# Kernel optimization log

Hardware: AMD Instinct MI355X
Metric: run time of the kernel (lower is better)

The kernel has to match this reference:

```python
import jax, jax.numpy as jnp
import numpy as np

N_NODES = 50000
IN_CH = 128
OUT_CH = 64
N_EDGES = 800000


def setup_inputs() -> dict:
    key = jax.random.key(0)
    k1, k2, k3, k4 = jax.random.split(key, 4)
    z = jax.random.normal(k1, (N_NODES, IN_CH), dtype=jnp.float32)
    edge_index = jax.random.randint(k2, (2, N_EDGES), 0, N_NODES, dtype=jnp.int64)
    # GCNConv params: weight [in, out] (glorot-ish), bias [out]
    W = jax.random.normal(k3, (IN_CH, OUT_CH), dtype=jnp.float32) / np.sqrt(IN_CH)
    b = jnp.zeros((OUT_CH,), dtype=jnp.float32)
    return {"z": z, "edge_index": edge_index, "W": W, "b": b}


def reference(z, edge_index, W, b):
    N = z.shape[0]
    # linear transform first (out_channels < in_channels reduces message traffic)
    x = z @ W  # [N, out]
    # add self-loops
    loop = jnp.arange(N, dtype=edge_index.dtype)
    src = jnp.concatenate([edge_index[0], loop])
    dst = jnp.concatenate([edge_index[1], loop])
    # symmetric normalization deg^-1/2 (degree counted on dst, incl. self-loops)
    deg = jnp.zeros((N,), dtype=x.dtype).at[dst].add(1.0)
    dinv = jnp.where(deg > 0, jax.lax.rsqrt(deg), 0.0)
    norm = dinv[src] * dinv[dst]  # [E+N]
    msg = x[src] * norm[:, None]  # gather + scale
    out = jax.ops.segment_sum(msg, dst, num_segments=N)  # scatter-add
    return jax.nn.relu(out + b)
```

## Files before the change

### kernel.cpp

```cpp
#include <hip/hip_runtime.h>
#include <hip/hip_bf16.h>

#define IN_CH 128
#define OUT_CH 64

#define CSHIFT 6
#define BNODES 64
#define NCMAX 1024
#define CAP 1536
#define BIN_EPT 8

typedef __attribute__((ext_vector_type(8))) short bf16x8;
typedef __attribute__((ext_vector_type(4))) float f32x4;

__device__ inline short f2bfs(float x) {
    __hip_bfloat16 h = __float2bfloat16(x);
    return __builtin_bit_cast(short, h);
}
__device__ inline float bf2f(unsigned short h) {
    unsigned int u = ((unsigned int)h) << 16;
    return __builtin_bit_cast(float, u);
}

__global__ void bin_edges(const int* __restrict__ ei, int* __restrict__ gctr,
                          unsigned int* __restrict__ ebuf, int E, int NC) {
    __shared__ int cnt[NCMAX];
    __shared__ int gbase[NCMAX];
    for (int i = threadIdx.x; i < NC; i += blockDim.x) cnt[i] = 0;
    __syncthreads();

    unsigned int pk[BIN_EPT];
    int bk[BIN_EPT];
    const int g0 = (blockIdx.x * blockDim.x + threadIdx.x) * BIN_EPT;

    if (g0 + BIN_EPT <= E) {
        int4 s0 = *(const int4*)(ei + g0);
        int4 s1 = *(const int4*)(ei + g0 + 4);
        int4 d0 = *(const int4*)(ei + E + g0);
        int4 d1 = *(const int4*)(ei + E + g0 + 4);
        int ss[BIN_EPT] = {s0.x, s0.y, s0.z, s0.w, s1.x, s1.y, s1.z, s1.w};
        int dd[BIN_EPT] = {d0.x, d0.y, d0.z, d0.w, d1.x, d1.y, d1.z, d1.w};
#pragma unroll
        for (int k = 0; k < BIN_EPT; ++k) {
            pk[k] = ((unsigned int)dd[k] << 16) | (unsigned int)ss[k];
            bk[k] = dd[k] >> CSHIFT;
            atomicAdd(&cnt[bk[k]], 1);
        }
    } else {
#pragma unroll
        for (int k = 0; k < BIN_EPT; ++k) {
            int e = g0 + k;
            if (e < E) {
                int s = ei[e];
                int d = ei[E + e];
                pk[k] = ((unsigned int)d << 16) | (unsigned int)s;
                bk[k] = d >> CSHIFT;
                atomicAdd(&cnt[bk[k]], 1);
            } else bk[k] = -1;
        }
    }
    __syncthreads();
    for (int i = threadIdx.x; i < NC; i += blockDim.x) {
        int c = cnt[i];
        gbase[i] = c ? atomicAdd(&gctr[i], c) : 0;
    }
    __syncthreads();
    for (int i = threadIdx.x; i < NC; i += blockDim.x) cnt[i] = 0;
    __syncthreads();
#pragma unroll
    for (int k = 0; k < BIN_EPT; ++k) {
        if (bk[k] >= 0) {
            int o = gbase[bk[k]] + atomicAdd(&cnt[bk[k]], 1);
            if (o < CAP)
                ebuf[(size_t)bk[k] * CAP + o] = pk[k];
        }
    }
}

__global__ void degree_wfrag(const unsigned int* __restrict__ ebuf,
                             const int* __restrict__ gctr,
                             float* __restrict__ dinv, int* __restrict__ boff,
                             int N, int NC,
                             const float* __restrict__ W,
                             unsigned short* __restrict__ wf) {
    const int b = blockIdx.x;
    if (b == NC) {
        for (int i = threadIdx.x; i < 4 * 4 * 64 * 8; i += blockDim.x) {
            int j    = i & 7;
            int lane = (i >> 3) & 63;
            int kk   = (i >> 9) & 3;
            int nt   = i >> 11;
            int k = kk * 32 + ((lane >> 4) & 3) * 8 + j;
            int n = nt * 16 + (lane & 15);
            wf[i] = (unsigned short)f2bfs(W[k * OUT_CH + n]);
        }
        return;
    }
    __shared__ int cnt[BNODES];
    __shared__ int off[BNODES];
    const int tid = threadIdx.x;
    const int n0 = b << CSHIFT;
    if (tid < BNODES) cnt[tid] = 0;
    __syncthreads();
    const int ecnt = min(gctr[b], CAP);
    const unsigned int* eb = ebuf + (size_t)b * CAP;
    for (int i = tid; i < ecnt; i += blockDim.x)
        atomicAdd(&cnt[(int)(eb[i] >> 16) - n0], 1);
    __syncthreads();
    if (tid < BNODES) off[tid] = cnt[tid];
    __syncthreads();
    for (int o = 1; o < BNODES; o <<= 1) {
        int v = 0;
        if (tid < BNODES && tid >= o) v = off[tid - o];
        __syncthreads();
        if (tid < BNODES) off[tid] += v;
        __syncthreads();
    }
    if (tid < BNODES) {
        boff[b * BNODES + tid] = off[tid] - cnt[tid];
        const int node = n0 + tid;
        if (node < N) dinv[node] = rsqrtf((float)(cnt[tid] + 1));
    }
}

__global__ void gemm_mfma(const float* __restrict__ z,
                          const unsigned short* __restrict__ wfrag,
                          const float* __restrict__ dinv,
                          unsigned short* __restrict__ y, int N) {
    const int lane = threadIdx.x & 63;
    const int wid  = threadIdx.x >> 6;
    const int row0 = blockIdx.x * 64 + wid * 16;

    bf16x8 bfr[4][4];
#pragma unroll
    for (int nt = 0; nt < 4; ++nt)
#pragma unroll
        for (int kk = 0; kk < 4; ++kk)
            bfr[nt][kk] = *(const bf16x8*)&wfrag[(((nt * 4 + kk) * 64) + lane) * 8];

    f32x4 acc[4];
#pragma unroll
    for (int nt = 0; nt < 4; ++nt) acc[nt] = (f32x4){0.f, 0.f, 0.f, 0.f};

    const int arow = row0 + (lane & 15);
    const int zrow = (arow < N) ? arow : (N - 1);
    const int sub  = lane >> 4;
    const float* zr = z + (size_t)zrow * IN_CH + sub * 8;

#pragma unroll
    for (int kk = 0; kk < 4; ++kk) {
        float4 f0 = *(const float4*)(zr + kk * 32);
        float4 f1 = *(const float4*)(zr + kk * 32 + 4);
        bf16x8 a;
        a[0] = f2bfs(f0.x); a[1] = f2bfs(f0.y);
        a[2] = f2bfs(f0.z); a[3] = f2bfs(f0.w);
        a[4] = f2bfs(f1.x); a[5] = f2bfs(f1.y);
        a[6] = f2bfs(f1.z); a[7] = f2bfs(f1.w);
#pragma unroll
        for (int nt = 0; nt < 4; ++nt)
            acc[nt] = __builtin_amdgcn_mfma_f32_16x16x32_bf16(a, bfr[nt][kk], acc[nt], 0, 0, 0);
    }

    const int crow0 = row0 + sub * 4;
#pragma unroll
    for (int r = 0; r < 4; ++r) {
        int row = crow0 + r;
        if (row < N) {
            float di = dinv[row];
#pragma unroll
            for (int nt = 0; nt < 4; ++nt)
                y[(size_t)row * OUT_CH + nt * 16 + (lane & 15)] =
                    (unsigned short)f2bfs(acc[nt][r] * di);
        }
    }
}

__global__ __launch_bounds__(512) void sort_gather(const unsigned int* __restrict__ ebuf,
                                                   const int* __restrict__ gctr,
                                                   const int* __restrict__ boff,
                                                   const unsigned int* __restrict__ y2,
                                                   const float* __restrict__ dinv,
                                                   const float* __restrict__ bias,
                                                   float* __restrict__ out, int N) {
    __shared__ unsigned short scol[CAP];
    __shared__ int off_s[BNODES];
    __shared__ int cur[BNODES];
    const int b = blockIdx.x;
    const int n0 = b << CSHIFT;
    const int tid = threadIdx.x;
    const int ecnt = min(gctr[b], CAP);
    const unsigned int* eb = ebuf + (size_t)b * CAP;

    if (tid < BNODES) {
        int o = boff[b * BNODES + tid];
        off_s[tid] = o;
        cur[tid] = o;
    }
    __syncthreads();

    for (int i = tid; i < ecnt; i += 512) {
        unsigned int p = eb[i];
        int rel = (int)(p >> 16) - n0;
        int slot = atomicAdd(&cur[rel], 1);
        scol[slot] = (unsigned short)(p & 0xFFFFu);
    }
    __syncthreads();

    const int lane = tid & 63;
    const int w = tid >> 6;
    const int half = lane >> 5;
    const int c2 = lane & 31;
    const float2 bv = *(const float2*)&bias[c2 * 2];

#pragma unroll
    for (int rnd = 0; rnd < 4; ++rnd) {
        const int nrel = rnd * 16 + w * 2 + half;
        const int node = n0 + nrel;
        const bool valid = node < N;
        int jbeg = valid ? off_s[nrel] : 0;
        int cend = valid ? ((nrel < BNODES - 1) ? off_s[nrel + 1] : ecnt) : 0;

        float accLo = 0.f, accHi = 0.f;
        if (valid) {
            unsigned int sv = y2[(size_t)node * 32 + c2];
            accLo = bf2f((unsigned short)(sv & 0xFFFFu));
            accHi = bf2f((unsigned short)(sv >> 16));
        }

        for (int j = jbeg; j < cend; j += 8) {
            unsigned int v[8]; bool m[8];
#pragma unroll
            for (int t = 0; t < 8; ++t) {
                int jj = j + t;
                m[t] = jj < cend;
                int s = scol[m[t] ? jj : (cend - 1)];
                v[t] = y2[(size_t)s * 32 + c2];
            }
#pragma unroll
            for (int t = 0; t < 8; ++t) {
                if (m[t]) {
                    accLo += bf2f((unsigned short)(v[t] & 0xFFFFu));
                    accHi += bf2f((unsigned short)(v[t] >> 16));
                }
            }
        }

        if (valid) {
            float di = dinv[node];
            float2 o2;
            o2.x = fmaxf(fmaf(accLo, di, bv.x), 0.f);
            o2.y = fmaxf(fmaf(accHi, di, bv.y), 0.f);
            *(float2*)&out[(size_t)node * OUT_CH + c2 * 2] = o2;
        }
    }
}

extern "C" void kernel_launch(void* const* d_in, const int* in_sizes, int n_in,
                              void* d_out, int out_size, void* d_ws, size_t ws_size,
                              hipStream_t stream) {
    const float* z  = (const float*)d_in[0];
    const int*   ei = (const int*)d_in[1];
    const float* W  = (const float*)d_in[2];
    const float* b  = (const float*)d_in[3];
    float*       out = (float*)d_out;

    const int N = in_sizes[0] / IN_CH;
    const int E = in_sizes[1] / 2;
    const int NC = (N + BNODES - 1) >> CSHIFT;

    unsigned short* y     = (unsigned short*)d_ws;
    unsigned int*   ebuf  = (unsigned int*)(y + (size_t)N * OUT_CH);
    float*          dinv  = (float*)(ebuf + (size_t)NC * CAP);
    int*            boff  = (int*)(dinv + N);
    int*            gctr  = boff + (size_t)NC * BNODES;
    unsigned short* wfrag = (unsigned short*)(((uintptr_t)(gctr + NC) + 15) & ~(uintptr_t)15);

    hipMemsetAsync(gctr, 0, (size_t)NC * sizeof(int), stream);

    const int binBlocks = (E + 256 * BIN_EPT - 1) / (256 * BIN_EPT);

    bin_edges   <<<binBlocks, 256, 0, stream>>>(ei, gctr, ebuf, E, NC);
    degree_wfrag<<<NC + 1, 256, 0, stream>>>(ebuf, gctr, dinv, boff, N, NC, W, wfrag);
    gemm_mfma   <<<(N + 63) / 64, 256, 0, stream>>>(z, wfrag, dinv, y, N);
    sort_gather <<<NC, 512, 0, stream>>>(ebuf, gctr, boff, (const unsigned int*)y,
                                         dinv, b, out, N);
}
```

Baseline: 71.57 us.

## Fuse degree/sort with GEMM and move W fragment prep into binning kernel

Merges the degree-count kernel and the GEMM into one per-bucket kernel that also counting-sorts edge columns into a global buffer. The weight-fragment conversion moves into an extra block of the binning kernel. The gather kernel then loads the presorted columns instead of re-sorting, and recomputes dinv from the CSR offsets instead of reading a dinv array. This drops one launch and one redundant atomic sort pass, at the cost of writing and reading a sorted-column buffer and a heavier fused kernel.

```diff
diff --git a/kernel.cpp b/kernel.cpp
--- a/kernel.cpp
+++ b/kernel.cpp
@@ -23,7 +23,20 @@
 }
 
 __global__ void bin_edges(const int* __restrict__ ei, int* __restrict__ gctr,
-                          unsigned int* __restrict__ ebuf, int E, int NC) {
+                          unsigned int* __restrict__ ebuf, int E, int NC, int nbin,
+                          const float* __restrict__ W, unsigned short* __restrict__ wf) {
+    if (blockIdx.x == (unsigned)nbin) {
+        for (int i = threadIdx.x; i < 4 * 4 * 64 * 8; i += blockDim.x) {
+            int j    = i & 7;
+            int lane = (i >> 3) & 63;
+            int kk   = (i >> 9) & 3;
+            int nt   = i >> 11;
+            int k = kk * 32 + ((lane >> 4) & 3) * 8 + j;
+            int n = nt * 16 + (lane & 15);
+            wf[i] = (unsigned short)f2bfs(W[k * OUT_CH + n]);
+        }
+        return;
+    }
     __shared__ int cnt[NCMAX];
     __shared__ int gbase[NCMAX];
     for (int i = threadIdx.x; i < NC; i += blockDim.x) cnt[i] = 0;
@@ -77,59 +90,63 @@
     }
 }
 
-__global__ void degree_wfrag(const unsigned int* __restrict__ ebuf,
-                             const int* __restrict__ gctr,
-                             float* __restrict__ dinv, int* __restrict__ boff,
-                             int N, int NC,
-                             const float* __restrict__ W,
-                             unsigned short* __restrict__ wf) {
-    const int b = blockIdx.x;
-    if (b == NC) {
-        for (int i = threadIdx.x; i < 4 * 4 * 64 * 8; i += blockDim.x) {
-            int j    = i & 7;
-            int lane = (i >> 3) & 63;
-            int kk   = (i >> 9) & 3;
-            int nt   = i >> 11;
-            int k = kk * 32 + ((lane >> 4) & 3) * 8 + j;
-            int n = nt * 16 + (lane & 15);
-            wf[i] = (unsigned short)f2bfs(W[k * OUT_CH + n]);
-        }
-        return;
-    }
+__global__ __launch_bounds__(256) void sort_gemm(const unsigned int* __restrict__ ebuf,
+                                                 const int* __restrict__ gctr,
+                                                 const float* __restrict__ z,
+                                                 const unsigned short* __restrict__ wfrag,
+                                                 int* __restrict__ boff,
+                                                 unsigned short* __restrict__ gscol,
+                                                 unsigned short* __restrict__ y, int N) {
+    __shared__ unsigned int epk[CAP];
+    __shared__ unsigned short scolL[CAP];
     __shared__ int cnt[BNODES];
     __shared__ int off[BNODES];
+    __shared__ float dinvL[BNODES];
+    const int b = blockIdx.x;
     const int tid = threadIdx.x;
     const int n0 = b << CSHIFT;
-    if (tid < BNODES) cnt[tid] = 0;
-    __syncthreads();
     const int ecnt = min(gctr[b], CAP);
     const unsigned int* eb = ebuf + (size_t)b * CAP;
-    for (int i = tid; i < ecnt; i += blockDim.x)
-        atomicAdd(&cnt[(int)(eb[i] >> 16) - n0], 1);
-    __syncthreads();
-    if (tid < BNODES) off[tid] = cnt[tid];
+
+    if (tid < BNODES) cnt[tid] = 0;
+    __syncthreads();
+    for (int i = tid; i < ecnt; i += 256) {
+        unsigned int p = eb[i];
+        epk[i] = p;
+        atomicAdd(&cnt[(int)(p >> 16) - n0], 1);
+    }
+    __syncthreads();
+
+    int deg = 0;
+    if (tid < BNODES) { deg = cnt[tid]; off[tid] = deg; }
     __syncthreads();
     for (int o = 1; o < BNODES; o <<= 1) {
-        int v = 0;
-        if (tid < BNODES && tid >= o) v = off[tid - o];
+        int v = (tid < BNODES && tid >= o) ? off[tid - o] : 0;
         __syncthreads();
         if (tid < BNODES) off[tid] += v;
         __syncthreads();
     }
     if (tid < BNODES) {
-        boff[b * BNODES + tid] = off[tid] - cnt[tid];
-        const int node = n0 + tid;
-        if (node < N) dinv[node] = rsqrtf((float)(cnt[tid] + 1));
-    }
-}
-
-__global__ void gemm_mfma(const float* __restrict__ z,
-                          const unsigned short* __restrict__ wfrag,
-                          const float* __restrict__ dinv,
-                          unsigned short* __restrict__ y, int N) {
-    const int lane = threadIdx.x & 63;
-    const int wid  = threadIdx.x >> 6;
-    const int row0 = blockIdx.x * 64 + wid * 16;
+        int ex = off[tid] - deg;
+        boff[b * BNODES + tid] = ex;
+        cnt[tid] = ex;
+        dinvL[tid] = rsqrtf((float)(deg + 1));
+    }
+    __syncthreads();
+
+    for (int i = tid; i < ecnt; i += 256) {
+        unsigned int p = epk[i];
+        int rel = (int)(p >> 16) - n0;
+        int slot = atomicAdd(&cnt[rel], 1);
+        scolL[slot] = (unsigned short)(p & 0xFFFFu);
+    }
+    __syncthreads();
+    for (int i = tid; i < ecnt; i += 256)
+        gscol[(size_t)b * CAP + i] = scolL[i];
+
+    const int lane = tid & 63;
+    const int wid  = tid >> 6;
+    const int row0 = n0 + wid * 16;
 
     bf16x8 bfr[4][4];
 #pragma unroll
@@ -161,12 +178,12 @@
             acc[nt] = __builtin_amdgcn_mfma_f32_16x16x32_bf16(a, bfr[nt][kk], acc[nt], 0, 0, 0);
     }
 
-    const int crow0 = row0 + sub * 4;
+    const int rrel0 = wid * 16 + sub * 4;
 #pragma unroll
     for (int r = 0; r < 4; ++r) {
-        int row = crow0 + r;
+        int row = n0 + rrel0 + r;
         if (row < N) {
-            float di = dinv[row];
+            float di = dinvL[rrel0 + r];
 #pragma unroll
             for (int nt = 0; nt < 4; ++nt)
                 y[(size_t)row * OUT_CH + nt * 16 + (lane & 15)] =
@@ -175,34 +192,26 @@
     }
 }
 
-__global__ __launch_bounds__(512) void sort_gather(const unsigned int* __restrict__ ebuf,
-                                                   const int* __restrict__ gctr,
-                                                   const int* __restrict__ boff,
-                                                   const unsigned int* __restrict__ y2,
-                                                   const float* __restrict__ dinv,
-                                                   const float* __restrict__ bias,
-                                                   float* __restrict__ out, int N) {
+__global__ __launch_bounds__(512) void gather(const int* __restrict__ gctr,
+                                              const int* __restrict__ boff,
+                                              const unsigned short* __restrict__ gscol,
+                                              const unsigned int* __restrict__ y2,
+                                              const float* __restrict__ bias,
+                                              float* __restrict__ out, int N) {
     __shared__ unsigned short scol[CAP];
-    __shared__ int off_s[BNODES];
-    __shared__ int cur[BNODES];
+    __shared__ int off_s[BNODES + 1];
     const int b = blockIdx.x;
     const int n0 = b << CSHIFT;
     const int tid = threadIdx.x;
     const int ecnt = min(gctr[b], CAP);
-    const unsigned int* eb = ebuf + (size_t)b * CAP;
-
-    if (tid < BNODES) {
-        int o = boff[b * BNODES + tid];
-        off_s[tid] = o;
-        cur[tid] = o;
-    }
-    __syncthreads();
-
-    for (int i = tid; i < ecnt; i += 512) {
-        unsigned int p = eb[i];
-        int rel = (int)(p >> 16) - n0;
-        int slot = atomicAdd(&cur[rel], 1);
-        scol[slot] = (unsigned short)(p & 0xFFFFu);
+
+    if (tid < BNODES) off_s[tid] = boff[b * BNODES + tid];
+    if (tid == 0) off_s[BNODES] = ecnt;
+    __syncthreads();
+    {
+        const unsigned int* gs32 = (const unsigned int*)(gscol + (size_t)b * CAP);
+        unsigned int* sc32 = (unsigned int*)scol;
+        for (int i = tid; i < (ecnt + 1) / 2; i += 512) sc32[i] = gs32[i];
     }
     __syncthreads();
 
@@ -218,7 +227,8 @@
         const int node = n0 + nrel;
         const bool valid = node < N;
         int jbeg = valid ? off_s[nrel] : 0;
-        int cend = valid ? ((nrel < BNODES - 1) ? off_s[nrel + 1] : ecnt) : 0;
+        int cend = valid ? off_s[nrel + 1] : 0;
+        const float di = rsqrtf((float)(cend - jbeg + 1));
 
         float accLo = 0.f, accHi = 0.f;
         if (valid) {
@@ -246,7 +256,6 @@
         }
 
         if (valid) {
-            float di = dinv[node];
             float2 o2;
             o2.x = fmaxf(fmaf(accLo, di, bv.x), 0.f);
             o2.y = fmaxf(fmaf(accHi, di, bv.y), 0.f);
@@ -270,8 +279,8 @@
 
     unsigned short* y     = (unsigned short*)d_ws;
     unsigned int*   ebuf  = (unsigned int*)(y + (size_t)N * OUT_CH);
-    float*          dinv  = (float*)(ebuf + (size_t)NC * CAP);
-    int*            boff  = (int*)(dinv + N);
+    unsigned short* gscol = (unsigned short*)(ebuf + (size_t)NC * CAP);
+    int*            boff  = (int*)(gscol + (size_t)NC * CAP);
     int*            gctr  = boff + (size_t)NC * BNODES;
     unsigned short* wfrag = (unsigned short*)(((uintptr_t)(gctr + NC) + 15) & ~(uintptr_t)15);
 
@@ -279,9 +288,7 @@
 
     const int binBlocks = (E + 256 * BIN_EPT - 1) / (256 * BIN_EPT);
 
-    bin_edges   <<<binBlocks, 256, 0, stream>>>(ei, gctr, ebuf, E, NC);
-    degree_wfrag<<<NC + 1, 256, 0, stream>>>(ebuf, gctr, dinv, boff, N, NC, W, wfrag);
-    gemm_mfma   <<<(N + 63) / 64, 256, 0, stream>>>(z, wfrag, dinv, y, N);
-    sort_gather <<<NC, 512, 0, stream>>>(ebuf, gctr, boff, (const unsigned int*)y,
-                                         dinv, b, out, N);
-}
+    bin_edges<<<binBlocks + 1, 256, 0, stream>>>(ei, gctr, ebuf, E, NC, binBlocks, W, wfrag);
+    sort_gemm<<<NC, 256, 0, stream>>>(ebuf, gctr, z, wfrag, boff, gscol, y, N);
+    gather   <<<NC, 512, 0, stream>>>(gctr, boff, gscol, (const unsigned int*)y, b, out, N);
+}
```

Measured after the change: 66.36 us. -7.3%, faster.
